# Kernel optimization log

Measured on AMD Instinct MI355X. Metric: run time of the kernel, lower is better.

Reference implementation:

```python
import jax, jax.numpy as jnp
import numpy as np

VOCAB = 50000
D = 256          # vector_dim == hidden size
SEQ = 128
BATCH = 4096
NUM_CLASSES = 5


def setup_inputs() -> dict:
    key = jax.random.key(0)
    ks = jax.random.split(key, 8)
    x = jax.random.randint(ks[0], (BATCH, SEQ), 0, VOCAB, dtype=jnp.int64)
    scale = 1.0 / np.sqrt(D)
    emb = jax.random.normal(ks[1], (VOCAB, D), dtype=jnp.float32)
    emb = emb.at[0].set(0.0)  # padding_idx=0 row is zero
    W_ih = jax.random.uniform(ks[2], (D, D), jnp.float32, -scale, scale)
    W_hh = jax.random.uniform(ks[3], (D, D), jnp.float32, -scale, scale)
    b_ih = jax.random.uniform(ks[4], (D,), jnp.float32, -scale, scale)
    b_hh = jax.random.uniform(ks[5], (D,), jnp.float32, -scale, scale)
    W_cls = jax.random.uniform(ks[6], (NUM_CLASSES, D), jnp.float32, -scale, scale)
    b_cls = jax.random.uniform(ks[7], (NUM_CLASSES,), jnp.float32, -scale, scale)
    return {"x": x, "emb": emb, "W_ih": W_ih, "W_hh": W_hh,
            "b_ih": b_ih, "b_hh": b_hh, "W_cls": W_cls, "b_cls": b_cls}


def reference(x, emb, W_ih, W_hh, b_ih, b_hh, W_cls, b_cls):
    # Embedding lookup: [B, S, D]
    xe = emb[x]
    # Precompute input projections for all timesteps in one GEMM.
    x_proj = jnp.einsum("bsd,hd->bsh", xe, W_ih) + b_ih + b_hh  # [B, S, D]

    def step(h, xp_t):
        h = jnp.tanh(xp_t + h @ W_hh.T)
        return h, None

    h0 = jnp.zeros((x.shape[0], W_hh.shape[0]), dtype=xe.dtype)
    # scan over time axis: [S, B, D]
    h_last, _ = jax.lax.scan(step, h0, jnp.swapaxes(x_proj, 0, 1))
    # classifier on last step
    return h_last @ W_cls.T + b_cls  # [B, 5]
```

## Files before the change

### kernel.cpp

```cpp
#include <hip/hip_runtime.h>


typedef __attribute__((ext_vector_type(8))) short bf16x8;
typedef __attribute__((ext_vector_type(4))) float f32x4;

#define VOCAB 50000
#define NBLK_EMB 256
#define LDS_STRIDE 264

__device__ __align__(256) unsigned short g_P[VOCAB * 256];

static __device__ __forceinline__ float bf2f(unsigned short u) {
    union { unsigned int i; float f; } v; v.i = ((unsigned int)u) << 16; return v.f;
}
static __device__ __forceinline__ float bfbits2f(unsigned int zext_u16) {
    union { unsigned int i; float f; } v; v.i = zext_u16 << 16; return v.f;
}
static __device__ __forceinline__ unsigned short f2bf_rne(float f) {
    union { float f; unsigned int i; } v; v.f = f;
    unsigned int r = v.i + 0x7FFFu + ((v.i >> 16) & 1u);
    return (unsigned short)(r >> 16);
}
static __device__ __forceinline__ unsigned short f2bf_fast(float f) {
    union { float f; unsigned int i; } v; v.f = f;
    return (unsigned short)((v.i + 0x8000u) >> 16);
}
static __device__ __forceinline__ bf16x8 cvt8(float4 a, float4 b) {
    bf16x8 r;
    r[0] = (short)f2bf_rne(a.x); r[1] = (short)f2bf_rne(a.y);
    r[2] = (short)f2bf_rne(a.z); r[3] = (short)f2bf_rne(a.w);
    r[4] = (short)f2bf_rne(b.x); r[5] = (short)f2bf_rne(b.y);
    r[6] = (short)f2bf_rne(b.z); r[7] = (short)f2bf_rne(b.w);
    return r;
}
static __device__ __forceinline__ bf16x8 load8_bf(const float* __restrict__ p) {
    return cvt8(((const float4*)p)[0], ((const float4*)p)[1]);
}
static __device__ __forceinline__ float fast_tanh(float x) {
    x = __builtin_amdgcn_fmed3f(x, -8.f, 8.f);
    float e = __expf(2.f * x);
    return __builtin_fmaf(-2.f, __builtin_amdgcn_rcpf(e + 1.f), 1.f);
}
static __device__ __forceinline__ void barrier_lds_only() {
    asm volatile("s_waitcnt lgkmcnt(0)\n\ts_barrier" ::: "memory");
}

__global__ __launch_bounds__(256)
void emb_proj_kernel(const float* __restrict__ emb,
                     const float* __restrict__ W_ih,
                     const float* __restrict__ b_ih,
                     const float* __restrict__ b_hh)
{
    __shared__ __align__(16) unsigned short tin [16 * LDS_STRIDE];
    __shared__ __align__(16) unsigned short tout[16 * LDS_STRIDE];
    const int tid  = threadIdx.x;
    const int lane = tid & 63;
    const int wid  = tid >> 6;
    const int n0   = wid * 64;
    const int row  = tid >> 4, seg = tid & 15;

    bf16x8 wf[4][8];
    float  bias[4];
    #pragma unroll
    for (int nt = 0; nt < 4; ++nt) {
        int n = n0 + nt * 16 + (lane & 15);
        bias[nt] = b_ih[n] + b_hh[n];
        #pragma unroll
        for (int kt = 0; kt < 8; ++kt)
            wf[nt][kt] = load8_bf(W_ih + n * 256 + (lane >> 4) * 8 + kt * 32);
    }

    int tile = blockIdx.x;
    float4 a0, a1, a2, a3;
    {
        const float4* s = (const float4*)(emb + ((size_t)tile * 16 + row) * 256 + seg * 16);
        a0 = s[0]; a1 = s[1]; a2 = s[2]; a3 = s[3];
    }

    for (; tile < 3125; tile += NBLK_EMB) {
        *(bf16x8*)(&tin[row * LDS_STRIDE + seg * 16])     = cvt8(a0, a1);
        *(bf16x8*)(&tin[row * LDS_STRIDE + seg * 16 + 8]) = cvt8(a2, a3);
        int tn = tile + NBLK_EMB;
        if (tn < 3125) {
            const float4* s = (const float4*)(emb + ((size_t)tn * 16 + row) * 256 + seg * 16);
            a0 = s[0]; a1 = s[1]; a2 = s[2]; a3 = s[3];
        }
        __syncthreads();

        f32x4 acc[4];
        #pragma unroll
        for (int nt = 0; nt < 4; ++nt) acc[nt] = (f32x4){0.f, 0.f, 0.f, 0.f};
        #pragma unroll
        for (int kt = 0; kt < 8; ++kt) {
            bf16x8 a = *(bf16x8*)(&tin[(lane & 15) * LDS_STRIDE + (lane >> 4) * 8 + kt * 32]);
            #pragma unroll
            for (int nt = 0; nt < 4; ++nt)
                acc[nt] = __builtin_amdgcn_mfma_f32_16x16x32_bf16(a, wf[nt][kt], acc[nt], 0, 0, 0);
        }
        #pragma unroll
        for (int nt = 0; nt < 4; ++nt) {
            int n = n0 + nt * 16 + (lane & 15);
            #pragma unroll
            for (int r = 0; r < 4; ++r)
                tout[((lane >> 4) * 4 + r) * LDS_STRIDE + n] = f2bf_rne(acc[nt][r] + bias[nt]);
        }
        __syncthreads();
        {
            uint4 o0 = *(uint4*)(&tout[row * LDS_STRIDE + seg * 16]);
            uint4 o1 = *(uint4*)(&tout[row * LDS_STRIDE + seg * 16 + 8]);
            uint4* dst = (uint4*)(g_P + ((size_t)tile * 16 + row) * 256 + seg * 16);
            dst[0] = o0; dst[1] = o1;
        }
    }
}

__global__ __launch_bounds__(512, 2)
void rnn_kernel(const int* __restrict__ x,
                const float* __restrict__ W_hh,
                const float* __restrict__ W_cls,
                const float* __restrict__ b_cls,
                float* __restrict__ out)
{
    __shared__ __align__(16) unsigned short h_lds[2][16 * 256];
    __shared__ __align__(16) int tok_t[128 * 16];
    __shared__ __align__(16) float wcls_lds[5 * 256];
    __shared__ float bcls_lds[5];

    const int tid  = threadIdx.x;
    const int lane = tid & 63;
    const int wid  = tid >> 6;
    const int b0   = blockIdx.x * 16;
    const int n0   = wid * 32;
    const int l15  = lane & 15;
    const int quad = lane >> 4;

    bf16x8 wf[2][8];
    #pragma unroll
    for (int nt = 0; nt < 2; ++nt) {
        int n = n0 + nt * 16 + l15;
        #pragma unroll
        for (int kt = 0; kt < 8; ++kt)
            wf[nt][kt] = load8_bf(W_hh + n * 256 + quad * 8 + kt * 32);
    }

    {
        int row = tid & 15, tq = tid >> 4;
        int4 v = *(const int4*)(x + (size_t)(b0 + row) * 128 + tq * 4);
        tok_t[(tq * 4 + 0) * 16 + row] = v.x;
        tok_t[(tq * 4 + 1) * 16 + row] = v.y;
        tok_t[(tq * 4 + 2) * 16 + row] = v.z;
        tok_t[(tq * 4 + 3) * 16 + row] = v.w;
    }
    if (tid < 320) ((float4*)wcls_lds)[tid] = ((const float4*)W_cls)[tid];
    if (tid < 5)   bcls_lds[tid] = b_cls[tid];
    #pragma unroll
    for (int i = 0; i < 4; ++i) ((unsigned int*)h_lds[0])[tid + i * 512] = 0;

    int aoff[8];
    #pragma unroll
    for (int kt = 0; kt < 8; ++kt)
        aoff[kt] = l15 * 512 + (((quad + 4 * kt) ^ l15) << 4);
    int woff[8];
    #pragma unroll
    for (int nt = 0; nt < 2; ++nt)
        #pragma unroll
        for (int r = 0; r < 4; ++r) {
            int row = quad * 4 + r;
            int g   = (n0 >> 3) + nt * 2 + (l15 >> 3);
            woff[nt * 4 + r] = row * 512 + ((g ^ row) << 4) + (l15 & 7) * 2;
        }

    const unsigned int colByte = (unsigned int)(n0 + l15) * 2;

    unsigned int gA[8], gB[8], gC[8], gD[8];
    #pragma unroll
    for (int r = 0; r < 4; ++r) {
        const int* xr = x + (size_t)(b0 + quad * 4 + r) * 128;
        const unsigned short* p0 = g_P + (size_t)xr[0] * 256 + n0 + l15;
        const unsigned short* p1 = g_P + (size_t)xr[1] * 256 + n0 + l15;
        const unsigned short* p2 = g_P + (size_t)xr[2] * 256 + n0 + l15;
        const unsigned short* p3 = g_P + (size_t)xr[3] * 256 + n0 + l15;
        gA[r] = p0[0]; gA[4 + r] = p0[16];
        gB[r] = p1[0]; gB[4 + r] = p1[16];
        gC[r] = p2[0]; gC[4 + r] = p2[16];
        gD[r] = p3[0]; gD[4 + r] = p3[16];
    }
    barrier_lds_only();

    char* const h0 = (char*)&h_lds[0][0];

    auto step = [&](const char* hA, char* hW, unsigned int* g, int t) {
        f32x4 acc0 = { bfbits2f(g[0]), bfbits2f(g[1]), bfbits2f(g[2]), bfbits2f(g[3]) };
        f32x4 acc1 = { bfbits2f(g[4]), bfbits2f(g[5]), bfbits2f(g[6]), bfbits2f(g[7]) };
        if (t + 4 < 128) {
            int4 tk = *(const int4*)&tok_t[(t + 4) * 16 + quad * 4];
            const unsigned short* r0 = (const unsigned short*)((const char*)g_P + ((unsigned int)tk.x * 512 + colByte));
            const unsigned short* r1 = (const unsigned short*)((const char*)g_P + ((unsigned int)tk.y * 512 + colByte));
            const unsigned short* r2 = (const unsigned short*)((const char*)g_P + ((unsigned int)tk.z * 512 + colByte));
            const unsigned short* r3 = (const unsigned short*)((const char*)g_P + ((unsigned int)tk.w * 512 + colByte));
            g[0] = r0[0]; g[4] = r0[16];
            g[1] = r1[0]; g[5] = r1[16];
            g[2] = r2[0]; g[6] = r2[16];
            g[3] = r3[0]; g[7] = r3[16];
        }
        #pragma unroll
        for (int kt = 0; kt < 8; ++kt) {
            bf16x8 a = *(const bf16x8*)(hA + aoff[kt]);
            acc0 = __builtin_amdgcn_mfma_f32_16x16x32_bf16(a, wf[0][kt], acc0, 0, 0, 0);
            acc1 = __builtin_amdgcn_mfma_f32_16x16x32_bf16(a, wf[1][kt], acc1, 0, 0, 0);
        }
        #pragma unroll
        for (int r = 0; r < 4; ++r) {
            *(unsigned short*)(hW + woff[r])     = f2bf_fast(fast_tanh(acc0[r]));
            *(unsigned short*)(hW + woff[4 + r]) = f2bf_fast(fast_tanh(acc1[r]));
        }
    };

    #pragma unroll 1
    for (int t4 = 0; t4 < 32; ++t4) {
        step(h0,        h0 + 8192, gA, 4 * t4);
        barrier_lds_only();
        step(h0 + 8192, h0,        gB, 4 * t4 + 1);
        barrier_lds_only();
        step(h0,        h0 + 8192, gC, 4 * t4 + 2);
        barrier_lds_only();
        step(h0 + 8192, h0,        gD, 4 * t4 + 3);
        barrier_lds_only();
    }

    if (tid < 320) {
        int q = tid & 3, p = tid >> 2;
        int row = p / 5, c = p - row * 5;
        float acc = 0.f;
        #pragma unroll
        for (int kk = 0; kk < 64; ++kk) {
            int k = q * 64 + kk;
            int off = row * 512 + ((((k >> 3) ^ row)) << 4) + (k & 7) * 2;
            acc += bf2f(*(const unsigned short*)(h0 + off)) * wcls_lds[c * 256 + k];
        }
        acc += __shfl_xor(acc, 1);
        acc += __shfl_xor(acc, 2);
        if (q == 0) out[(size_t)(b0 + row) * 5 + c] = acc + bcls_lds[c];
    }
}

extern "C" void kernel_launch(void* const* d_in, const int* in_sizes, int n_in,
                              void* d_out, int out_size, void* d_ws, size_t ws_size,
                              hipStream_t stream)
{
    const int*   x     = (const int*)d_in[0];
    const float* emb   = (const float*)d_in[1];
    const float* W_ih  = (const float*)d_in[2];
    const float* W_hh  = (const float*)d_in[3];
    const float* b_ih  = (const float*)d_in[4];
    const float* b_hh  = (const float*)d_in[5];
    const float* W_cls = (const float*)d_in[6];
    const float* b_cls = (const float*)d_in[7];
    float*       out   = (float*)d_out;
    (void)d_ws; (void)ws_size;

    emb_proj_kernel<<<NBLK_EMB, 256, 0, stream>>>(emb, W_ih, b_ih, b_hh);
    rnn_kernel<<<256, 512, 0, stream>>>(x, W_hh, W_cls, b_cls, out);
}
```

Before: 226.2 us.

## Fuse embedding projection and RNN into one cooperative kernel with grid sync

Merges the vocabulary-wide embedding projection kernel and the recurrent kernel into a single cooperative launch. Each block first projects its share of the vocabulary tiles into the bf16 table, double-buffering LDS across two tiles, and writes results straight to global memory without an LDS staging pass. A grid-wide sync follows, and then the block runs the recurrence. This removes one kernel launch and its tail gap, at the cost of a grid barrier and a cooperative launch, with the 512-thread blocks now also doing the projection work.

```diff
diff --git a/kernel.cpp b/kernel.cpp
--- a/kernel.cpp
+++ b/kernel.cpp
@@ -1,11 +1,13 @@
 #include <hip/hip_runtime.h>
+#include <hip/hip_cooperative_groups.h>
+
+namespace cg = cooperative_groups;
 
 
 typedef __attribute__((ext_vector_type(8))) short bf16x8;
 typedef __attribute__((ext_vector_type(4))) float f32x4;
 
 #define VOCAB 50000
-#define NBLK_EMB 256
 #define LDS_STRIDE 264
 
 __device__ __align__(256) unsigned short g_P[VOCAB * 256];
@@ -45,82 +47,18 @@
     asm volatile("s_waitcnt lgkmcnt(0)\n\ts_barrier" ::: "memory");
 }
 
-__global__ __launch_bounds__(256)
-void emb_proj_kernel(const float* __restrict__ emb,
-                     const float* __restrict__ W_ih,
-                     const float* __restrict__ b_ih,
-                     const float* __restrict__ b_hh)
+__global__ __launch_bounds__(512, 2)
+void rnn_fused_kernel(const int* __restrict__ x,
+                      const float* __restrict__ emb,
+                      const float* __restrict__ W_ih,
+                      const float* __restrict__ W_hh,
+                      const float* __restrict__ b_ih,
+                      const float* __restrict__ b_hh,
+                      const float* __restrict__ W_cls,
+                      const float* __restrict__ b_cls,
+                      float* __restrict__ out)
 {
-    __shared__ __align__(16) unsigned short tin [16 * LDS_STRIDE];
-    __shared__ __align__(16) unsigned short tout[16 * LDS_STRIDE];
-    const int tid  = threadIdx.x;
-    const int lane = tid & 63;
-    const int wid  = tid >> 6;
-    const int n0   = wid * 64;
-    const int row  = tid >> 4, seg = tid & 15;
-
-    bf16x8 wf[4][8];
-    float  bias[4];
-    #pragma unroll
-    for (int nt = 0; nt < 4; ++nt) {
-        int n = n0 + nt * 16 + (lane & 15);
-        bias[nt] = b_ih[n] + b_hh[n];
-        #pragma unroll
-        for (int kt = 0; kt < 8; ++kt)
-            wf[nt][kt] = load8_bf(W_ih + n * 256 + (lane >> 4) * 8 + kt * 32);
-    }
-
-    int tile = blockIdx.x;
-    float4 a0, a1, a2, a3;
-    {
-        const float4* s = (const float4*)(emb + ((size_t)tile * 16 + row) * 256 + seg * 16);
-        a0 = s[0]; a1 = s[1]; a2 = s[2]; a3 = s[3];
-    }
-
-    for (; tile < 3125; tile += NBLK_EMB) {
-        *(bf16x8*)(&tin[row * LDS_STRIDE + seg * 16])     = cvt8(a0, a1);
-        *(bf16x8*)(&tin[row * LDS_STRIDE + seg * 16 + 8]) = cvt8(a2, a3);
-        int tn = tile + NBLK_EMB;
-        if (tn < 3125) {
-            const float4* s = (const float4*)(emb + ((size_t)tn * 16 + row) * 256 + seg * 16);
-            a0 = s[0]; a1 = s[1]; a2 = s[2]; a3 = s[3];
-        }
-        __syncthreads();
-
-        f32x4 acc[4];
-        #pragma unroll
-        for (int nt = 0; nt < 4; ++nt) acc[nt] = (f32x4){0.f, 0.f, 0.f, 0.f};
-        #pragma unroll
-        for (int kt = 0; kt < 8; ++kt) {
-            bf16x8 a = *(bf16x8*)(&tin[(lane & 15) * LDS_STRIDE + (lane >> 4) * 8 + kt * 32]);
-            #pragma unroll
-            for (int nt = 0; nt < 4; ++nt)
-                acc[nt] = __builtin_amdgcn_mfma_f32_16x16x32_bf16(a, wf[nt][kt], acc[nt], 0, 0, 0);
-        }
-        #pragma unroll
-        for (int nt = 0; nt < 4; ++nt) {
-            int n = n0 + nt * 16 + (lane & 15);
-            #pragma unroll
-            for (int r = 0; r < 4; ++r)
-                tout[((lane >> 4) * 4 + r) * LDS_STRIDE + n] = f2bf_rne(acc[nt][r] + bias[nt]);
-        }
-        __syncthreads();
-        {
-            uint4 o0 = *(uint4*)(&tout[row * LDS_STRIDE + seg * 16]);
-            uint4 o1 = *(uint4*)(&tout[row * LDS_STRIDE + seg * 16 + 8]);
-            uint4* dst = (uint4*)(g_P + ((size_t)tile * 16 + row) * 256 + seg * 16);
-            dst[0] = o0; dst[1] = o1;
-        }
-    }
-}
-
-__global__ __launch_bounds__(512, 2)
-void rnn_kernel(const int* __restrict__ x,
-                const float* __restrict__ W_hh,
-                const float* __restrict__ W_cls,
-                const float* __restrict__ b_cls,
-                float* __restrict__ out)
-{
+    __shared__ __align__(16) unsigned short tin[2][16 * LDS_STRIDE];
     __shared__ __align__(16) unsigned short h_lds[2][16 * 256];
     __shared__ __align__(16) int tok_t[128 * 16];
     __shared__ __align__(16) float wcls_lds[5 * 256];
@@ -129,19 +67,11 @@
     const int tid  = threadIdx.x;
     const int lane = tid & 63;
     const int wid  = tid >> 6;
-    const int b0   = blockIdx.x * 16;
+    const int b    = blockIdx.x;
+    const int b0   = b * 16;
     const int n0   = wid * 32;
     const int l15  = lane & 15;
     const int quad = lane >> 4;
-
-    bf16x8 wf[2][8];
-    #pragma unroll
-    for (int nt = 0; nt < 2; ++nt) {
-        int n = n0 + nt * 16 + l15;
-        #pragma unroll
-        for (int kt = 0; kt < 8; ++kt)
-            wf[nt][kt] = load8_bf(W_hh + n * 256 + quad * 8 + kt * 32);
-    }
 
     {
         int row = tid & 15, tq = tid >> 4;
@@ -155,6 +85,77 @@
     if (tid < 5)   bcls_lds[tid] = b_cls[tid];
     #pragma unroll
     for (int i = 0; i < 4; ++i) ((unsigned int*)h_lds[0])[tid + i * 512] = 0;
+
+    {
+        bf16x8 wfA[2][8];
+        float  biasA[2];
+        #pragma unroll
+        for (int nt = 0; nt < 2; ++nt) {
+            int n = n0 + nt * 16 + l15;
+            biasA[nt] = b_ih[n] + b_hh[n];
+            #pragma unroll
+            for (int kt = 0; kt < 8; ++kt)
+                wfA[nt][kt] = load8_bf(W_ih + n * 256 + quad * 8 + kt * 32);
+        }
+
+        const int srow = tid >> 5, sseg = tid & 31;
+        float4 p0a, p0b, p1a, p1b;
+        {
+            const float4* s0 = (const float4*)(emb + ((size_t)b * 16 + srow) * 256 + sseg * 8);
+            p0a = s0[0]; p0b = s0[1];
+            int t1 = b + 256;
+            if (t1 < 3125) {
+                const float4* s1 = (const float4*)(emb + ((size_t)t1 * 16 + srow) * 256 + sseg * 8);
+                p1a = s1[0]; p1b = s1[1];
+            }
+        }
+
+        #define PROJ_STEP(I, PA, PB, TBUF)                                                 \
+        {                                                                                  \
+            int tile = b + (I) * 256;                                                      \
+            if (tile < 3125) {                                                             \
+                *(bf16x8*)(&TBUF[srow * LDS_STRIDE + sseg * 8]) = cvt8(PA, PB);            \
+                int tf = tile + 512;                                                       \
+                if (tf < 3125) {                                                           \
+                    const float4* s = (const float4*)(emb + ((size_t)tf * 16 + srow) * 256 + sseg * 8); \
+                    PA = s[0]; PB = s[1];                                                  \
+                }                                                                          \
+                barrier_lds_only();                                                        \
+                f32x4 acc0 = (f32x4){0.f, 0.f, 0.f, 0.f};                                  \
+                f32x4 acc1 = (f32x4){0.f, 0.f, 0.f, 0.f};                                  \
+                _Pragma("unroll")                                                          \
+                for (int kt = 0; kt < 8; ++kt) {                                           \
+                    bf16x8 a = *(bf16x8*)(&TBUF[l15 * LDS_STRIDE + quad * 8 + kt * 32]);   \
+                    acc0 = __builtin_amdgcn_mfma_f32_16x16x32_bf16(a, wfA[0][kt], acc0, 0, 0, 0); \
+                    acc1 = __builtin_amdgcn_mfma_f32_16x16x32_bf16(a, wfA[1][kt], acc1, 0, 0, 0); \
+                }                                                                          \
+                unsigned short* prow = g_P + ((size_t)tile * 16 + quad * 4) * 256 + n0;    \
+                _Pragma("unroll")                                                          \
+                for (int r = 0; r < 4; ++r) {                                              \
+                    prow[r * 256 + l15]      = f2bf_rne(acc0[r] + biasA[0]);               \
+                    prow[r * 256 + 16 + l15] = f2bf_rne(acc1[r] + biasA[1]);               \
+                }                                                                          \
+            }                                                                              \
+        }
+
+        #pragma unroll 1
+        for (int i2 = 0; i2 < 7; ++i2) {
+            PROJ_STEP(2 * i2,     p0a, p0b, tin[0]);
+            PROJ_STEP(2 * i2 + 1, p1a, p1b, tin[1]);
+        }
+        #undef PROJ_STEP
+    }
+
+    cg::this_grid().sync();
+
+    bf16x8 wfh[2][8];
+    #pragma unroll
+    for (int nt = 0; nt < 2; ++nt) {
+        int n = n0 + nt * 16 + l15;
+        #pragma unroll
+        for (int kt = 0; kt < 8; ++kt)
+            wfh[nt][kt] = load8_bf(W_hh + n * 256 + quad * 8 + kt * 32);
+    }
 
     int aoff[8];
     #pragma unroll
@@ -206,8 +207,8 @@
         #pragma unroll
         for (int kt = 0; kt < 8; ++kt) {
             bf16x8 a = *(const bf16x8*)(hA + aoff[kt]);
-            acc0 = __builtin_amdgcn_mfma_f32_16x16x32_bf16(a, wf[0][kt], acc0, 0, 0, 0);
-            acc1 = __builtin_amdgcn_mfma_f32_16x16x32_bf16(a, wf[1][kt], acc1, 0, 0, 0);
+            acc0 = __builtin_amdgcn_mfma_f32_16x16x32_bf16(a, wfh[0][kt], acc0, 0, 0, 0);
+            acc1 = __builtin_amdgcn_mfma_f32_16x16x32_bf16(a, wfh[1][kt], acc1, 0, 0, 0);
         }
         #pragma unroll
         for (int r = 0; r < 4; ++r) {
@@ -259,6 +260,9 @@
     float*       out   = (float*)d_out;
     (void)d_ws; (void)ws_size;
 
-    emb_proj_kernel<<<NBLK_EMB, 256, 0, stream>>>(emb, W_ih, b_ih, b_hh);
-    rnn_kernel<<<256, 512, 0, stream>>>(x, W_hh, W_cls, b_cls, out);
-}
+    void* args[] = { (void*)&x, (void*)&emb, (void*)&W_ih, (void*)&W_hh,
+                     (void*)&b_ih, (void*)&b_hh, (void*)&W_cls, (void*)&b_cls,
+                     (void*)&out };
+    hipLaunchCooperativeKernel((const void*)rnn_fused_kernel,
+                               dim3(256), dim3(512), args, 0, stream);
+}
```

Result: slower. 294.1 us (+30.0%).
